# Performance work log

Measured on AMD Instinct MI355X. Metric: run time of the kernel, lower is better.

## Reference

```python
import jax, jax.numpy as jnp
import numpy as np

B, H, W, C = 8, 28, 28, 1024
NH = 16
HD = C // NH          # head dim 64
HID = 4 * C           # mlp hidden 4096
BC = C // 2           # bottleneck channels 512
SCALE = HD ** -0.5


def setup_inputs() -> dict:
    key = jax.random.key(0)
    ks = iter(jax.random.split(key, 32))
    def rn(shape, s=0.02):
        return jax.random.normal(next(ks), shape, jnp.float32) * s
    return dict(
        x=jax.random.normal(next(ks), (B, H, W, C), jnp.float32),
        norm1_w=jnp.ones((C,), jnp.float32), norm1_b=jnp.zeros((C,), jnp.float32),
        qkv_w=rn((C, 3 * C)), qkv_b=jnp.zeros((3 * C,), jnp.float32),
        proj_w=rn((C, C)), proj_b=jnp.zeros((C,), jnp.float32),
        rel_h=rn((2 * H - 1, HD)), rel_w=rn((2 * W - 1, HD)),
        norm2_w=jnp.ones((C,), jnp.float32), norm2_b=jnp.zeros((C,), jnp.float32),
        fc1_w=rn((C, HID)), fc1_b=jnp.zeros((HID,), jnp.float32),
        fc2_w=rn((HID, C)), fc2_b=jnp.zeros((C,), jnp.float32),
        conv1_w=rn((1, 1, C, BC)), ln1_w=jnp.ones((BC,), jnp.float32), ln1_b=jnp.zeros((BC,), jnp.float32),
        conv2_w=rn((3, 3, BC, BC)), ln2_w=jnp.ones((BC,), jnp.float32), ln2_b=jnp.zeros((BC,), jnp.float32),
        conv3_w=rn((1, 1, BC, C)), ln3_w=rn((C,)), ln3_b=rn((C,)),
    )


def _ln(x, w, b, eps):
    # layernorm over last axis (channels in NHWC)
    m = jnp.mean(x, -1, keepdims=True)
    v = jnp.mean((x - m) ** 2, -1, keepdims=True)
    return (x - m) * jax.lax.rsqrt(v + eps) * w + b


def _conv(x, w, pad):
    return jax.lax.conv_general_dilated(
        x, w, (1, 1), pad, dimension_numbers=('NHWC', 'HWIO', 'NHWC'))


def _gelu(x):
    return jax.nn.gelu(x, approximate=False)


def _block_forward(x, norm1_w, norm1_b, qkv_w, qkv_b, proj_w, proj_b,
                   rel_h, rel_w, norm2_w, norm2_b, fc1_w, fc1_b, fc2_w, fc2_b,
                   conv1_w, ln1_w, ln1_b, conv2_w, ln2_w, ln2_b, conv3_w, ln3_w, ln3_b):
    S = H * W
    shortcut = x
    xn = _ln(x, norm1_w, norm1_b, 1e-5)

    # ---- attention with decomposed relative position bias ----
    qkv = xn.reshape(B, S, C) @ qkv_w + qkv_b                 # [B,S,3C]
    qkv = qkv.reshape(B, S, 3, NH, HD).transpose(2, 0, 3, 1, 4)  # [3,B,nh,S,hd]
    q, k, v = qkv[0], qkv[1], qkv[2]
    attn = jnp.einsum('bnsd,bntd->bnst', q * SCALE, k)        # [B,nh,S,S]

    idx_h = jnp.arange(H)[:, None] - jnp.arange(H)[None, :] + (H - 1)
    idx_w = jnp.arange(W)[:, None] - jnp.arange(W)[None, :] + (W - 1)
    Rh = rel_h[idx_h]   # [H,H,hd]
    Rw = rel_w[idx_w]   # [W,W,hd]
    qr = q.reshape(B, NH, H, W, HD)
    bias_h = jnp.einsum('bnhwd,hkd->bnhwk', qr, Rh)           # [B,nh,H,W,H]
    bias_w = jnp.einsum('bnhwd,wkd->bnhwk', qr, Rw)           # [B,nh,H,W,W]
    attn = (attn.reshape(B, NH, H, W, H, W)
            + bias_h[..., :, None] + bias_w[..., None, :]).reshape(B, NH, S, S)

    attn = jax.nn.softmax(attn, axis=-1)
    out = jnp.einsum('bnst,bntd->bnsd', attn, v)              # [B,nh,S,hd]
    out = out.transpose(0, 2, 1, 3).reshape(B, H, W, C)
    out = out @ proj_w + proj_b

    x = shortcut + out

    # ---- MLP ----
    xn = _ln(x, norm2_w, norm2_b, 1e-5)
    x = x + (_gelu(xn.reshape(B, S, C) @ fc1_w + fc1_b) @ fc2_w + fc2_b).reshape(B, H, W, C)

    # ---- residual bottleneck conv (channel LayerNorm, eps=1e-6) ----
    out = _conv(x, conv1_w, 'VALID')
    out = _gelu(_ln(out, ln1_w, ln1_b, 1e-6))
    out = _conv(out, conv2_w, ((1, 1), (1, 1)))
    out = _gelu(_ln(out, ln2_w, ln2_b, 1e-6))
    out = _conv(out, conv3_w, 'VALID')
    out = _ln(out, ln3_w, ln3_b, 1e-6)
    return x + out


def reference(x, norm1_w, norm1_b, qkv_w, qkv_b, proj_w, proj_b,
              rel_h, rel_w, norm2_w, norm2_b, fc1_w, fc1_b, fc2_w, fc2_b,
              conv1_w, ln1_w, ln1_b, conv2_w, ln2_w, ln2_b, conv3_w, ln3_w, ln3_b):
    return _block_forward(x, norm1_w, norm1_b, qkv_w, qkv_b, proj_w, proj_b,
                          rel_h, rel_w, norm2_w, norm2_b, fc1_w, fc1_b, fc2_w, fc2_b,
                          conv1_w, ln1_w, ln1_b, conv2_w, ln2_w, ln2_b, conv3_w, ln3_w, ln3_b)
```

## Files before the change

### kernel.cpp

```cpp
#include <hip/hip_runtime.h>
#include <cstdint>
#include <cstddef>

using u16 = unsigned short;
using u32 = unsigned int;

__device__ __forceinline__ float bf2f(u16 u){
  union { u32 i; float f; } x; x.i = ((u32)u) << 16; return x.f;
}
__device__ __forceinline__ u16 f2bf(float f){
  union { float f; u32 i; } x; x.f = f;
  u32 r = x.i + 0x7fffu + ((x.i >> 16) & 1u);
  return (u16)(r >> 16);
}
__device__ __forceinline__ float gelu_f(float x){
  return 0.5f * x * (1.0f + erff(x * 0.70710678118654752f));
}
__device__ __forceinline__ void gld16(const void* g, void* l){
  __builtin_amdgcn_global_load_lds((__attribute__((address_space(1))) void*)(void*)g,
                                   (__attribute__((address_space(3))) void*)l, 16, 0, 0);
}

typedef __bf16 bf16x8 __attribute__((ext_vector_type(8)));
typedef float  f32x4  __attribute__((ext_vector_type(4)));
typedef u16    u16x4  __attribute__((ext_vector_type(4)));

__global__ __launch_bounds__(256) void k_transpose(const float* __restrict__ src,
                                                   u16* __restrict__ dst, int R, int C){
  __shared__ u16 tile[32][33];
  int bx = blockIdx.x * 32;
  int by = blockIdx.y * 32;
  int tx = threadIdx.x & 31;
  int ty = threadIdx.x >> 5;
  for (int r = ty; r < 32; r += 8)
    tile[r][tx] = f2bf(src[(size_t)(by + r) * C + bx + tx]);
  __syncthreads();
  for (int r = ty; r < 32; r += 8)
    dst[(size_t)(bx + r) * R + by + tx] = tile[tx][r];
}

template<bool IN_F32, bool DO_GELU>
__global__ __launch_bounds__(256) void k_layernorm(const void* __restrict__ inp,
    const float* __restrict__ w, const float* __restrict__ bsh,
    u16* __restrict__ out, int cols, float eps){
  int row = blockIdx.x, t = threadIdx.x;
  size_t base = (size_t)row * cols;
  const float* inf = (const float*)inp;
  const u16*  inb = (const u16*)inp;
  float v[4];
  int ep = cols >> 8;
  float s = 0.f, ss = 0.f;
  for (int e = 0; e < ep; ++e){
    int idx = t + (e << 8);
    float x = IN_F32 ? inf[base + idx] : bf2f(inb[base + idx]);
    v[e] = x; s += x; ss += x * x;
  }
#pragma unroll
  for (int off = 1; off < 64; off <<= 1){
    s  += __shfl_xor(s, off, 64);
    ss += __shfl_xor(ss, off, 64);
  }
  __shared__ float red[8];
  int wv = t >> 6;
  if ((t & 63) == 0){ red[wv] = s; red[4 + wv] = ss; }
  __syncthreads();
  s  = red[0] + red[1] + red[2] + red[3];
  ss = red[4] + red[5] + red[6] + red[7];
  float inv = 1.f / (float)cols;
  float mean = s * inv;
  float var = ss * inv - mean * mean;
  float rs = rsqrtf(var + eps);
  for (int e = 0; e < ep; ++e){
    int idx = t + (e << 8);
    float y = (v[e] - mean) * rs * w[idx] + bsh[idx];
    if (DO_GELU) y = gelu_f(y);
    out[base + idx] = f2bf(y);
  }
}

__global__ __launch_bounds__(256) void k_final(const u16* __restrict__ c3,
    const u16* __restrict__ x2, const float* __restrict__ w,
    const float* __restrict__ bsh, float* __restrict__ out){
  int row = blockIdx.x, t = threadIdx.x;
  size_t base = (size_t)row << 10;
  float v[4];
  float s = 0.f, ss = 0.f;
#pragma unroll
  for (int e = 0; e < 4; ++e){
    int idx = t + (e << 8);
    float x = bf2f(c3[base + idx]);
    v[e] = x; s += x; ss += x * x;
  }
#pragma unroll
  for (int off = 1; off < 64; off <<= 1){
    s  += __shfl_xor(s, off, 64);
    ss += __shfl_xor(ss, off, 64);
  }
  __shared__ float red[8];
  int wv = t >> 6;
  if ((t & 63) == 0){ red[wv] = s; red[4 + wv] = ss; }
  __syncthreads();
  s  = red[0] + red[1] + red[2] + red[3];
  ss = red[4] + red[5] + red[6] + red[7];
  float mean = s * (1.f/1024.f);
  float var = ss * (1.f/1024.f) - mean * mean;
  float rs = rsqrtf(var + 1e-6f);
#pragma unroll
  for (int e = 0; e < 4; ++e){
    int idx = t + (e << 8);
    float y = (v[e] - mean) * rs * w[idx] + bsh[idx];
    out[base + idx] = bf2f(x2[base + idx]) + y;
  }
}

template<bool BIAS, bool GELU, bool RES, bool OUTB, bool OUTF>
__global__ __launch_bounds__(256, 2) void k_gemm(
    const u16* __restrict__ A, const u16* __restrict__ Bt,
    const float* __restrict__ bias, const float* __restrict__ resf,
    u16* __restrict__ outb, float* __restrict__ outf, int N, int K)
{
  __shared__ __align__(16) u16 As[128 * 32];
  __shared__ __align__(16) u16 Bs[128 * 32];
  int t = threadIdx.x, lane = t & 63, wv = t >> 6;
  int m0 = blockIdx.y << 7, n0 = blockIdx.x << 7;
  int wm = (wv >> 1) << 6, wn = (wv & 1) << 6;

  f32x4 acc[4][4];
  const f32x4 z4 = {0.f, 0.f, 0.f, 0.f};
#pragma unroll
  for (int i = 0; i < 4; ++i)
#pragma unroll
    for (int j = 0; j < 4; ++j) acc[i][j] = z4;

  int srow = (wv << 5) + (lane >> 2);
  int skp  = (lane & 3) << 3;
  const u16* Ag = A  + (size_t)(m0 + srow) * K + skp;
  const u16* Bg = Bt + (size_t)(n0 + srow) * K + skp;
  u16* As0 = &As[(wv << 5) * 32];
  u16* As1 = As0 + 16 * 32;
  u16* Bs0 = &Bs[(wv << 5) * 32];
  u16* Bs1 = Bs0 + 16 * 32;
  const size_t rowskip = (size_t)16 * K;

  int fr = lane & 15, fq = (lane >> 4) << 3;

  for (int k0 = 0; k0 < K; k0 += 32){
    gld16(Ag + k0, As0);
    gld16(Ag + rowskip + k0, As1);
    gld16(Bg + k0, Bs0);
    gld16(Bg + rowskip + k0, Bs1);
    __syncthreads();
    bf16x8 af[4], bfr[4];
#pragma unroll
    for (int i = 0; i < 4; ++i)
      af[i] = *(const bf16x8*)&As[(wm + i * 16 + fr) * 32 + fq];
#pragma unroll
    for (int j = 0; j < 4; ++j)
      bfr[j] = *(const bf16x8*)&Bs[(wn + j * 16 + fr) * 32 + fq];
#pragma unroll
    for (int i = 0; i < 4; ++i)
#pragma unroll
      for (int j = 0; j < 4; ++j)
        acc[i][j] = __builtin_amdgcn_mfma_f32_16x16x32_bf16(af[i], bfr[j], acc[i][j], 0, 0, 0);
    __syncthreads();
  }

  int rr = (lane >> 4) << 2;
  int cc = lane & 15;
#pragma unroll
  for (int i = 0; i < 4; ++i)
#pragma unroll
    for (int j = 0; j < 4; ++j){
      int gc = n0 + wn + j * 16 + cc;
      float bb = BIAS ? bias[gc] : 0.f;
#pragma unroll
      for (int r = 0; r < 4; ++r){
        int gr = m0 + wm + i * 16 + rr + r;
        size_t idx = (size_t)gr * N + gc;
        float vv = acc[i][j][r] + bb;
        if (RES) vv += resf[idx];
        if (GELU) vv = gelu_f(vv);
        if (OUTF) outf[idx] = vv;
        if (OUTB) outb[idx] = f2bf(vv);
      }
    }
}

__global__ __launch_bounds__(256) void k_vtrans(const u16* __restrict__ qkv, u16* __restrict__ vtg){
  __shared__ u32 tile[64][33];
  int bnh = blockIdx.x;
  int st  = blockIdx.y;
  int b = bnh >> 4, nh = bnh & 15;
  int t = threadIdx.x;
  int tx = t & 31;
  int ty = t >> 5;
  const u16* src = qkv + (size_t)b * 784 * 3072 + 2048 + nh * 64;
  int s0 = st << 6;
  for (int r = ty; r < 64; r += 8){
    int s = s0 + r;
    u32 val = 0u;
    if (s < 784) val = *(const u32*)(src + (size_t)s * 3072 + tx * 2);
    tile[r][tx] = val;
  }
  __syncthreads();
  u16* dst = vtg + (size_t)bnh * 64 * 832 + s0;
  for (int d = ty; d < 64; d += 8){
    u32 lo = tile[2 * tx][d >> 1];
    u32 hi = tile[2 * tx + 1][d >> 1];
    u16 a  = (d & 1) ? (u16)(lo >> 16) : (u16)lo;
    u16 bb = (d & 1) ? (u16)(hi >> 16) : (u16)hi;
    u32 pk = (u32)a | ((u32)bb << 16);
    *(u32*)(dst + (size_t)d * 832 + 2 * tx) = pk;
  }
}

#define ATT_STR 72
#define GSTR 132
__global__ __launch_bounds__(256, 4) void k_attn4(const u16* __restrict__ qkv,
    const float* __restrict__ relh, const float* __restrict__ relw,
    const u16* __restrict__ vtg, u16* __restrict__ out)
{
  __shared__ __align__(16) u16 p_s[128 * ATT_STR];
  __shared__ __align__(16) u16 gh_t[28 * GSTR];
  __shared__ __align__(16) u16 gw_t[28 * GSTR];

  const int t = threadIdx.x, lane = t & 63, wv = t >> 6;
  int id = blockIdx.x;
  int xr = id & 7, rest = id >> 3;
  int qt = rest % 7, gg = rest / 7;
  int bnh = xr + (gg << 3);
  const int b = bnh >> 4, nh = bnh & 15;
  const int q0 = qt << 7;
  const size_t rowbase = (size_t)b * 784;
  const int wq0 = wv << 5;
  const int fr = lane & 15;
  const int fq = lane >> 4;

  u16* rh_s = p_s;
  u16* rw_s = p_s + 64 * ATT_STR;
  {
    int row = t >> 2, c0 = (t & 3) << 4;
    u16 bh_[16], bw_[16];
    if (row < 55){
      const float* ph = relh + row * 64 + c0;
      const float* pw = relw + row * 64 + c0;
#pragma unroll
      for (int e = 0; e < 16; ++e){ bh_[e] = f2bf(ph[e]); bw_[e] = f2bf(pw[e]); }
    } else {
#pragma unroll
      for (int e = 0; e < 16; ++e){ bh_[e] = 0; bw_[e] = 0; }
    }
    *(uint4*)&rh_s[row * ATT_STR + c0]     = *(uint4*)bh_;
    *(uint4*)&rh_s[row * ATT_STR + c0 + 8] = *(uint4*)(bh_ + 8);
    *(uint4*)&rw_s[row * ATT_STR + c0]     = *(uint4*)bw_;
    *(uint4*)&rw_s[row * ATT_STR + c0 + 8] = *(uint4*)(bw_ + 8);
  }

  bf16x8 qf[2][2];
#pragma unroll
  for (int mf = 0; mf < 2; ++mf)
#pragma unroll
    for (int ks = 0; ks < 2; ++ks){
      int row = q0 + wq0 + mf * 16 + fr;
      if (row < 784){
        qf[mf][ks] = *(const bf16x8*)(qkv + (rowbase + row) * 3072 + nh * 64 + fq * 8 + ks * 32);
      } else {
        uint4 z = {0u,0u,0u,0u}; qf[mf][ks] = *(bf16x8*)&z;
      }
    }
  __syncthreads();

  const f32x4 z4 = {0.f,0.f,0.f,0.f};
#pragma unroll
  for (int which = 0; which < 2; ++which){
    const u16* rs = which ? rw_s : rh_s;
    f32x4 G[2][4];
#pragma unroll
    for (int mf = 0; mf < 2; ++mf)
#pragma unroll
      for (int nf = 0; nf < 4; ++nf) G[mf][nf] = z4;
#pragma unroll
    for (int nf = 0; nf < 4; ++nf){
      bf16x8 rf0 = *(const bf16x8*)&rs[(nf * 16 + fr) * ATT_STR + fq * 8];
      bf16x8 rf1 = *(const bf16x8*)&rs[(nf * 16 + fr) * ATT_STR + fq * 8 + 32];
#pragma unroll
      for (int mf = 0; mf < 2; ++mf){
        G[mf][nf] = __builtin_amdgcn_mfma_f32_16x16x32_bf16(qf[mf][0], rf0, G[mf][nf], 0, 0, 0);
        G[mf][nf] = __builtin_amdgcn_mfma_f32_16x16x32_bf16(qf[mf][1], rf1, G[mf][nf], 0, 0, 0);
      }
    }
    u16* gt = which ? gw_t : gh_t;
#pragma unroll
    for (int mf = 0; mf < 2; ++mf)
#pragma unroll
      for (int r = 0; r < 4; ++r){
        int lr = wq0 + mf * 16 + fq * 4 + r;
        int grow = q0 + lr;
        int hq = grow / 28;
        int coord = which ? (grow - hq * 28) : hq;
#pragma unroll
        for (int nf = 0; nf < 4; ++nf){
          int j = nf * 16 + fr;
          int kk = coord + 27 - j;
          if ((unsigned)kk < 28u) gt[kk * GSTR + lr] = f2bf(G[mf][nf][r]);
        }
      }
  }
  __syncthreads();

  f32x4 acc[2][5];
#pragma unroll
  for (int mf = 0; mf < 2; ++mf)
#pragma unroll
    for (int nf = 0; nf < 5; ++nf) acc[mf][nf] = z4;

  u16 onesu[8];
#pragma unroll
  for (int e = 0; e < 8; ++e) onesu[e] = 0x3f80;
  bf16x8 onesf = *(bf16x8*)onesu;

  const u16* kgb = qkv + rowbase * 3072 + 1024 + nh * 64 + fq * 8;
  const u16* vgb = vtg + ((size_t)bnh * 64 + fr) * 832 + fq * 8;

  for (int kt = 0; kt < 13; ++kt){
    const int ktb = kt << 6;
    f32x4 S[2][4];
#pragma unroll
    for (int nf = 0; nf < 4; ++nf){
      int jg = ktb + nf * 16 + fr;
      int jc = jg < 784 ? jg : 783;
      const u16* kp = kgb + (size_t)jc * 3072;
      bf16x8 kf0 = *(const bf16x8*)kp;
      bf16x8 kf1 = *(const bf16x8*)(kp + 32);
#pragma unroll
      for (int mf = 0; mf < 2; ++mf){
        f32x4 s = z4;
        s = __builtin_amdgcn_mfma_f32_16x16x32_bf16(qf[mf][0], kf0, s, 0, 0, 0);
        s = __builtin_amdgcn_mfma_f32_16x16x32_bf16(qf[mf][1], kf1, s, 0, 0, 0);
        S[mf][nf] = s;
      }
    }

    int hj[4], wj[4]; bool val[4];
#pragma unroll
    for (int nf = 0; nf < 4; ++nf){
      int jg = ktb + nf * 16 + fr;
      int h = jg / 28;
      hj[nf] = h; wj[nf] = jg - h * 28; val[nf] = (jg < 784);
    }

#pragma unroll
    for (int mf = 0; mf < 2; ++mf){
      int lrb = wq0 + mf * 16 + fq * 4;
#pragma unroll
      for (int nf = 0; nf < 4; ++nf){
        u16x4 h4 = *(const u16x4*)&gh_t[hj[nf] * GSTR + lrb];
        u16x4 w4 = *(const u16x4*)&gw_t[wj[nf] * GSTR + lrb];
#pragma unroll
        for (int r = 0; r < 4; ++r){
          float p = 0.f;
          if (val[nf])
            p = __expf(fmaf(0.125f, S[mf][nf][r], bf2f(h4[r]) + bf2f(w4[r])));
          p_s[(lrb + r) * ATT_STR + nf * 16 + fr] = f2bf(p);
        }
      }
    }

#pragma unroll
    for (int ks = 0; ks < 2; ++ks){
      bf16x8 pf0 = *(const bf16x8*)&p_s[(wq0 + fr) * ATT_STR + fq * 8 + ks * 32];
      bf16x8 pf1 = *(const bf16x8*)&p_s[(wq0 + 16 + fr) * ATT_STR + fq * 8 + ks * 32];
#pragma unroll
      for (int nf = 0; nf < 4; ++nf){
        bf16x8 vf = *(const bf16x8*)(vgb + (size_t)(nf * 16) * 832 + ktb + ks * 32);
        acc[0][nf] = __builtin_amdgcn_mfma_f32_16x16x32_bf16(pf0, vf, acc[0][nf], 0, 0, 0);
        acc[1][nf] = __builtin_amdgcn_mfma_f32_16x16x32_bf16(pf1, vf, acc[1][nf], 0, 0, 0);
      }
      acc[0][4] = __builtin_amdgcn_mfma_f32_16x16x32_bf16(pf0, onesf, acc[0][4], 0, 0, 0);
      acc[1][4] = __builtin_amdgcn_mfma_f32_16x16x32_bf16(pf1, onesf, acc[1][4], 0, 0, 0);
    }
  }

#pragma unroll
  for (int mf = 0; mf < 2; ++mf)
#pragma unroll
    for (int r = 0; r < 4; ++r){
      int row = q0 + wq0 + mf * 16 + fq * 4 + r;
      if (row < 784){
        float inv = 1.f / acc[mf][4][r];
        u16* dp = out + (rowbase + row) * 1024 + nh * 64 + fr;
#pragma unroll
        for (int nf = 0; nf < 4; ++nf)
          dp[nf * 16] = f2bf(acc[mf][nf][r] * inv);
      }
    }
}

__global__ __launch_bounds__(256) void k_im2col(const u16* __restrict__ g, u16* __restrict__ im){
  int idx = blockIdx.x * 256 + threadIdx.x;
  int p  = idx / 576;
  int c8 = idx - p * 576;
  int k0 = c8 << 3;
  int t9 = k0 >> 9;
  int ci = k0 & 511;
  int ky = t9 / 3, kx = t9 - ky * 3;
  int bb = p / 784;
  int s = p - bb * 784;
  int h = s / 28, w = s - h * 28;
  int hh = h + ky - 1, ww = w + kx - 1;
  uint4 val = make_uint4(0u, 0u, 0u, 0u);
  if ((unsigned)hh < 28u && (unsigned)ww < 28u)
    val = *(const uint4*)&g[(((size_t)(bb * 28 + hh)) * 28 + ww) * 512 + ci];
  *(uint4*)&im[(size_t)p * 4608 + k0] = val;
}

extern "C" void kernel_launch(void* const* d_in, const int* in_sizes, int n_in,
                              void* d_out, int out_size, void* d_ws, size_t ws_size,
                              hipStream_t stream)
{
  (void)in_sizes; (void)n_in; (void)out_size; (void)ws_size;
  const float* x      = (const float*)d_in[0];
  const float* n1w    = (const float*)d_in[1];
  const float* n1b    = (const float*)d_in[2];
  const float* qkv_w  = (const float*)d_in[3];
  const float* qkv_b  = (const float*)d_in[4];
  const float* proj_w = (const float*)d_in[5];
  const float* proj_b = (const float*)d_in[6];
  const float* rel_h  = (const float*)d_in[7];
  const float* rel_w  = (const float*)d_in[8];
  const float* n2w    = (const float*)d_in[9];
  const float* n2b    = (const float*)d_in[10];
  const float* fc1_w  = (const float*)d_in[11];
  const float* fc1_b  = (const float*)d_in[12];
  const float* fc2_w  = (const float*)d_in[13];
  const float* fc2_b  = (const float*)d_in[14];
  const float* c1w    = (const float*)d_in[15];
  const float* l1w    = (const float*)d_in[16];
  const float* l1b    = (const float*)d_in[17];
  const float* c2w    = (const float*)d_in[18];
  const float* l2w    = (const float*)d_in[19];
  const float* l2b    = (const float*)d_in[20];
  const float* c3w    = (const float*)d_in[21];
  const float* l3w    = (const float*)d_in[22];
  const float* l3b    = (const float*)d_in[23];

  char* ws = (char*)d_ws;
  size_t off = 0;
  auto alloc = [&](size_t bytes) -> void* {
    void* p = ws + off; off += (bytes + 255) & ~(size_t)255; return p;
  };
  const size_t M = 6272;
  u16* qkvT  = (u16*)alloc((size_t)3072 * 1024 * 2);
  u16* projT = (u16*)alloc((size_t)1024 * 1024 * 2);
  u16* fc1T  = (u16*)alloc((size_t)4096 * 1024 * 2);
  u16* fc2T  = (u16*)alloc((size_t)1024 * 4096 * 2);
  u16* c1T   = (u16*)alloc((size_t)512 * 1024 * 2);
  u16* c2T   = (u16*)alloc((size_t)512 * 4608 * 2);
  u16* c3T   = (u16*)alloc((size_t)1024 * 512 * 2);
  u16* qkvbuf = (u16*)alloc(M * 3072 * 2);
  u16* attn   = (u16*)alloc(M * 1024 * 2);
  u16* xn     = (u16*)alloc(M * 1024 * 2);
  float* x1   = (float*)alloc(M * 1024 * 4);
  u16* x2b    = (u16*)alloc(M * 1024 * 2);
  u16* c1buf  = (u16*)alloc(M * 512 * 2);
  u16* g1buf  = (u16*)alloc(M * 512 * 2);
  u16* hmlp   = qkvbuf;
  u16* im     = qkvbuf;
  u16* xn2    = xn;
  u16* c2buf  = c1buf;
  u16* g2buf  = g1buf;
  u16* c3buf  = attn;
  u16* vtg    = (u16*)x1;

  dim3 blk(256);
  k_transpose<<<dim3(3072/32, 1024/32), blk, 0, stream>>>(qkv_w, qkvT, 1024, 3072);
  k_transpose<<<dim3(1024/32, 1024/32), blk, 0, stream>>>(proj_w, projT, 1024, 1024);
  k_transpose<<<dim3(4096/32, 1024/32), blk, 0, stream>>>(fc1_w, fc1T, 1024, 4096);
  k_transpose<<<dim3(1024/32, 4096/32), blk, 0, stream>>>(fc2_w, fc2T, 4096, 1024);
  k_transpose<<<dim3(512/32, 1024/32),  blk, 0, stream>>>(c1w, c1T, 1024, 512);
  k_transpose<<<dim3(512/32, 4608/32),  blk, 0, stream>>>(c2w, c2T, 4608, 512);
  k_transpose<<<dim3(1024/32, 512/32),  blk, 0, stream>>>(c3w, c3T, 512, 1024);

  k_layernorm<true,false><<<6272, blk, 0, stream>>>(x, n1w, n1b, xn, 1024, 1e-5f);
  k_gemm<true,false,false,true,false><<<dim3(24,49), blk, 0, stream>>>(
      xn, qkvT, qkv_b, nullptr, qkvbuf, nullptr, 3072, 1024);
  k_vtrans<<<dim3(128, 13), blk, 0, stream>>>(qkvbuf, vtg);
  k_attn4<<<896, blk, 0, stream>>>(qkvbuf, rel_h, rel_w, vtg, attn);
  k_gemm<true,false,true,false,true><<<dim3(8,49), blk, 0, stream>>>(
      attn, projT, proj_b, x, nullptr, x1, 1024, 1024);
  k_layernorm<true,false><<<6272, blk, 0, stream>>>(x1, n2w, n2b, xn2, 1024, 1e-5f);
  k_gemm<true,true,false,true,false><<<dim3(32,49), blk, 0, stream>>>(
      xn2, fc1T, fc1_b, nullptr, hmlp, nullptr, 4096, 1024);
  k_gemm<true,false,true,true,false><<<dim3(8,49), blk, 0, stream>>>(
      hmlp, fc2T, fc2_b, x1, x2b, nullptr, 1024, 4096);
  k_gemm<false,false,false,true,false><<<dim3(4,49), blk, 0, stream>>>(
      x2b, c1T, nullptr, nullptr, c1buf, nullptr, 512, 1024);
  k_layernorm<false,true><<<6272, blk, 0, stream>>>(c1buf, l1w, l1b, g1buf, 512, 1e-6f);
  k_im2col<<<14112, blk, 0, stream>>>(g1buf, im);
  k_gemm<false,false,false,true,false><<<dim3(4,49), blk, 0, stream>>>(
      im, c2T, nullptr, nullptr, c2buf, nullptr, 512, 4608);
  k_layernorm<false,true><<<6272, blk, 0, stream>>>(c2buf, l2w, l2b, g2buf, 512, 1e-6f);
  k_gemm<false,false,false,true,false><<<dim3(8,49), blk, 0, stream>>>(
      g2buf, c3T, nullptr, nullptr, c3buf, nullptr, 1024, 512);
  k_final<<<6272, blk, 0, stream>>>(c3buf, x2b, l3w, l3b, (float*)d_out);
}
```

Before: 757.4 us.

## Stage K/V tiles in swizzled LDS for attention and remap GEMM blocks per XCD

The attention kernel now stages each 64-key K and V tile into XOR-swizzled shared memory with global_load_lds. Before, every wave read K and V directly from global memory, so the four waves fetched the same data redundantly. The softmax exponent switches to exp2f, with log2(e) folded into the scale and the bias tables. The GEMM remaps workgroup indices so that contiguous output tiles land on the same XCD, which should improve L2 reuse. The cost is two extra barriers per key tile and more shared memory, which lowers the occupancy target from 4 to 3 blocks per CU.

```diff
diff --git a/kernel.cpp b/kernel.cpp
--- a/kernel.cpp
+++ b/kernel.cpp
@@ -122,7 +122,17 @@
   __shared__ __align__(16) u16 As[128 * 32];
   __shared__ __align__(16) u16 Bs[128 * 32];
   int t = threadIdx.x, lane = t & 63, wv = t >> 6;
-  int m0 = blockIdx.y << 7, n0 = blockIdx.x << 7;
+
+  int nbx = gridDim.x;
+  int nwg = nbx * gridDim.y;
+  int li  = blockIdx.y * nbx + blockIdx.x;
+  int qc = nwg >> 3, rc = nwg & 7;
+  int xcd = li & 7, jj = li >> 3;
+  int wg = (xcd < rc ? xcd * (qc + 1) : rc * (qc + 1) + (xcd - rc) * qc) + jj;
+  int byy = wg / nbx;
+  int bxx = wg - byy * nbx;
+  int m0 = byy << 7, n0 = bxx << 7;
+
   int wm = (wv >> 1) << 6, wn = (wv & 1) << 6;
 
   f32x4 acc[4][4];
@@ -214,13 +224,16 @@
   }
 }
 
-#define ATT_STR 72
+#define PST 72
 #define GSTR 132
-__global__ __launch_bounds__(256, 4) void k_attn4(const u16* __restrict__ qkv,
+#define LOG2E 1.4426950408889634f
+__global__ __launch_bounds__(256, 3) void k_attn7(const u16* __restrict__ qkv,
     const float* __restrict__ relh, const float* __restrict__ relw,
     const u16* __restrict__ vtg, u16* __restrict__ out)
 {
-  __shared__ __align__(16) u16 p_s[128 * ATT_STR];
+  __shared__ __align__(16) u16 k_s[64 * 64];
+  __shared__ __align__(16) u16 v_s[64 * 64];
+  __shared__ __align__(16) u16 p_s[128 * PST];
   __shared__ __align__(16) u16 gh_t[28 * GSTR];
   __shared__ __align__(16) u16 gw_t[28 * GSTR];
 
@@ -237,7 +250,7 @@
   const int fq = lane >> 4;
 
   u16* rh_s = p_s;
-  u16* rw_s = p_s + 64 * ATT_STR;
+  u16* rw_s = p_s + 64 * PST;
   {
     int row = t >> 2, c0 = (t & 3) << 4;
     u16 bh_[16], bw_[16];
@@ -250,10 +263,10 @@
 #pragma unroll
       for (int e = 0; e < 16; ++e){ bh_[e] = 0; bw_[e] = 0; }
     }
-    *(uint4*)&rh_s[row * ATT_STR + c0]     = *(uint4*)bh_;
-    *(uint4*)&rh_s[row * ATT_STR + c0 + 8] = *(uint4*)(bh_ + 8);
-    *(uint4*)&rw_s[row * ATT_STR + c0]     = *(uint4*)bw_;
-    *(uint4*)&rw_s[row * ATT_STR + c0 + 8] = *(uint4*)(bw_ + 8);
+    *(uint4*)&rh_s[row * PST + c0]     = *(uint4*)bh_;
+    *(uint4*)&rh_s[row * PST + c0 + 8] = *(uint4*)(bh_ + 8);
+    *(uint4*)&rw_s[row * PST + c0]     = *(uint4*)bw_;
+    *(uint4*)&rw_s[row * PST + c0 + 8] = *(uint4*)(bw_ + 8);
   }
 
   bf16x8 qf[2][2];
@@ -281,8 +294,8 @@
       for (int nf = 0; nf < 4; ++nf) G[mf][nf] = z4;
 #pragma unroll
     for (int nf = 0; nf < 4; ++nf){
-      bf16x8 rf0 = *(const bf16x8*)&rs[(nf * 16 + fr) * ATT_STR + fq * 8];
-      bf16x8 rf1 = *(const bf16x8*)&rs[(nf * 16 + fr) * ATT_STR + fq * 8 + 32];
+      bf16x8 rf0 = *(const bf16x8*)&rs[(nf * 16 + fr) * PST + fq * 8];
+      bf16x8 rf1 = *(const bf16x8*)&rs[(nf * 16 + fr) * PST + fq * 8 + 32];
 #pragma unroll
       for (int mf = 0; mf < 2; ++mf){
         G[mf][nf] = __builtin_amdgcn_mfma_f32_16x16x32_bf16(qf[mf][0], rf0, G[mf][nf], 0, 0, 0);
@@ -302,7 +315,7 @@
         for (int nf = 0; nf < 4; ++nf){
           int j = nf * 16 + fr;
           int kk = coord + 27 - j;
-          if ((unsigned)kk < 28u) gt[kk * GSTR + lr] = f2bf(G[mf][nf][r]);
+          if ((unsigned)kk < 28u) gt[kk * GSTR + lr] = f2bf(G[mf][nf][r] * LOG2E);
         }
       }
   }
@@ -319,19 +332,38 @@
   for (int e = 0; e < 8; ++e) onesu[e] = 0x3f80;
   bf16x8 onesf = *(bf16x8*)onesu;
 
-  const u16* kgb = qkv + rowbase * 3072 + 1024 + nh * 64 + fq * 8;
-  const u16* vgb = vtg + ((size_t)bnh * 64 + fr) * 832 + fq * 8;
+  const int sr = lane >> 3;
+  const int sc = (lane & 7) ^ sr;
+  const u16* kstage = qkv + rowbase * 3072 + 1024 + nh * 64;
+  const u16* vstage = vtg + (size_t)bnh * 64 * 832;
+  const int r0 = (wv << 4) + sr;
+  u16* kd0 = &k_s[(wv << 4) * 64];
+  u16* kd1 = &k_s[((wv << 4) + 8) * 64];
+  u16* vd0 = &v_s[(wv << 4) * 64];
+  u16* vd1 = &v_s[((wv << 4) + 8) * 64];
+  const int swz = (fr & 7);
+
+  const float SSC = 0.125f * LOG2E;
 
   for (int kt = 0; kt < 13; ++kt){
     const int ktb = kt << 6;
+    __syncthreads();
+    {
+      int jg0 = ktb + r0;       int jc0 = jg0 < 784 ? jg0 : 783;
+      int jg1 = jg0 + 8;        int jc1 = jg1 < 784 ? jg1 : 783;
+      gld16(kstage + (size_t)jc0 * 3072 + (sc << 3), kd0);
+      gld16(kstage + (size_t)jc1 * 3072 + (sc << 3), kd1);
+      gld16(vstage + (size_t)r0 * 832 + ktb + (sc << 3), vd0);
+      gld16(vstage + (size_t)(r0 + 8) * 832 + ktb + (sc << 3), vd1);
+    }
+    __syncthreads();
+
     f32x4 S[2][4];
 #pragma unroll
     for (int nf = 0; nf < 4; ++nf){
-      int jg = ktb + nf * 16 + fr;
-      int jc = jg < 784 ? jg : 783;
-      const u16* kp = kgb + (size_t)jc * 3072;
-      bf16x8 kf0 = *(const bf16x8*)kp;
-      bf16x8 kf1 = *(const bf16x8*)(kp + 32);
+      int rb = (nf * 16 + fr) << 6;
+      bf16x8 kf0 = *(const bf16x8*)&k_s[rb + ((fq ^ swz) << 3)];
+      bf16x8 kf1 = *(const bf16x8*)&k_s[rb + (((fq + 4) ^ swz) << 3)];
 #pragma unroll
       for (int mf = 0; mf < 2; ++mf){
         f32x4 s = z4;
@@ -360,19 +392,19 @@
         for (int r = 0; r < 4; ++r){
           float p = 0.f;
           if (val[nf])
-            p = __expf(fmaf(0.125f, S[mf][nf][r], bf2f(h4[r]) + bf2f(w4[r])));
-          p_s[(lrb + r) * ATT_STR + nf * 16 + fr] = f2bf(p);
+            p = exp2f(fmaf(SSC, S[mf][nf][r], bf2f(h4[r]) + bf2f(w4[r])));
+          p_s[(lrb + r) * PST + nf * 16 + fr] = f2bf(p);
         }
       }
     }
 
 #pragma unroll
     for (int ks = 0; ks < 2; ++ks){
-      bf16x8 pf0 = *(const bf16x8*)&p_s[(wq0 + fr) * ATT_STR + fq * 8 + ks * 32];
-      bf16x8 pf1 = *(const bf16x8*)&p_s[(wq0 + 16 + fr) * ATT_STR + fq * 8 + ks * 32];
+      bf16x8 pf0 = *(const bf16x8*)&p_s[(wq0 + fr) * PST + fq * 8 + ks * 32];
+      bf16x8 pf1 = *(const bf16x8*)&p_s[(wq0 + 16 + fr) * PST + fq * 8 + ks * 32];
 #pragma unroll
       for (int nf = 0; nf < 4; ++nf){
-        bf16x8 vf = *(const bf16x8*)(vgb + (size_t)(nf * 16) * 832 + ktb + ks * 32);
+        bf16x8 vf = *(const bf16x8*)&v_s[((nf * 16 + fr) << 6) + (((fq + ks * 4) ^ swz) << 3)];
         acc[0][nf] = __builtin_amdgcn_mfma_f32_16x16x32_bf16(pf0, vf, acc[0][nf], 0, 0, 0);
         acc[1][nf] = __builtin_amdgcn_mfma_f32_16x16x32_bf16(pf1, vf, acc[1][nf], 0, 0, 0);
       }
@@ -485,7 +517,7 @@
   k_gemm<true,false,false,true,false><<<dim3(24,49), blk, 0, stream>>>(
       xn, qkvT, qkv_b, nullptr, qkvbuf, nullptr, 3072, 1024);
   k_vtrans<<<dim3(128, 13), blk, 0, stream>>>(qkvbuf, vtg);
-  k_attn4<<<896, blk, 0, stream>>>(qkvbuf, rel_h, rel_w, vtg, attn);
+  k_attn7<<<896, blk, 0, stream>>>(qkvbuf, rel_h, rel_w, vtg, attn);
   k_gemm<true,false,true,false,true><<<dim3(8,49), blk, 0, stream>>>(
       attn, projT, proj_b, x, nullptr, x1, 1024, 1024);
   k_layernorm<true,false><<<6272, blk, 0, stream>>>(x1, n2w, n2b, xn2, 1024, 1e-5f);
```

Measured after the change: 725.6 us. 4.2% less time.
